# Performance work log

Measured on AMD Instinct MI355X. Metric: run time of the kernel, lower is better.

## Reference

```python
import jax, jax.numpy as jnp
import numpy as np

ALPHA = 0.2  # leaky relu slope
NEG_BIG = -9e15


def setup_inputs() -> dict:
    key = jax.random.key(0)
    k1, k2, k3, k4 = jax.random.split(key, 4)
    B, N, Fin, Fout = 8, 2048, 128, 128
    h = jax.random.normal(k1, (B, N, Fin), dtype=jnp.float32)
    adj = jax.random.randint(k2, (N, N), 0, 2, dtype=jnp.int32)
    # xavier_uniform with gain=1.414
    limW = 1.414 * np.sqrt(6.0 / (Fin + Fout))
    W = jax.random.uniform(k3, (Fin, Fout), minval=-limW, maxval=limW, dtype=jnp.float32)
    lima = 1.414 * np.sqrt(6.0 / (2 * Fout + 1))
    a = jax.random.uniform(k4, (2 * Fout, 1), minval=-lima, maxval=lima, dtype=jnp.float32)
    return {"h": h, "adj": adj, "W": W, "a": a}


def reference(h, adj, W, a):
    # Wh: [B, N, F]
    Wh = jnp.einsum("bnf,fo->bno", h, W)
    Fout = W.shape[1]
    a1, a2 = a[:Fout, 0], a[Fout:, 0]  # [F], [F]
    # Additive score decomposition (same math as concat trick):
    # e[b,i,j] = leakyrelu(Wh_i . a1 + Wh_j . a2)
    s1 = Wh @ a1  # [B, N] (source/query part)
    s2 = Wh @ a2  # [B, N] (target part)
    e = s1[:, :, None] + s2[:, None, :]  # [B, N, N]
    e = jnp.where(e > 0, e, ALPHA * e)   # leaky relu
    e = jnp.where(adj[None, :, :] > 0, e, NEG_BIG)
    attention = jax.nn.softmax(e, axis=2)  # [B, N, N]
    # dropout is identity in eval mode
    h_prime = jnp.einsum("bij,bjf->bif", attention, Wh)
    return h_prime
```

## Files before the change

### kernel.cpp

```cpp
#include <hip/hip_runtime.h>
#include <hip/hip_bf16.h>
#include <stdint.h>

#define ALPHA 0.2f

typedef __attribute__((ext_vector_type(8))) short bf16x8;
typedef __attribute__((ext_vector_type(4))) float f32x4;

__device__ __forceinline__ short f2bf(float f) {
    union { float f; uint32_t u; } c; c.f = f;
    uint32_t u = c.u + 0x7FFF + ((c.u >> 16) & 1);
    return (short)(u >> 16);
}

__device__ __forceinline__ uint32_t pk_bf16(float lo, float hi) {
    union { float f; uint32_t u; } a, b;
    a.f = lo; b.f = hi;
    return __builtin_amdgcn_perm(b.u + 0x8000u, a.u + 0x8000u, 0x07060302u);
}

__global__ __launch_bounds__(256) void pack_adj_kernel(
        const int* __restrict__ adj, uint8_t* __restrict__ bytes,
        const float* __restrict__ W, short* __restrict__ WTg) {
    int t = blockIdx.x * 256 + threadIdx.x;
    const int4* a4 = reinterpret_cast<const int4*>(adj) + (size_t)t * 2;
    int4 x0 = a4[0], x1 = a4[1];
    uint32_t m = 0;
    m |= (x0.x > 0) ? 1u   : 0u;  m |= (x0.y > 0) ? 2u   : 0u;
    m |= (x0.z > 0) ? 4u   : 0u;  m |= (x0.w > 0) ? 8u   : 0u;
    m |= (x1.x > 0) ? 16u  : 0u;  m |= (x1.y > 0) ? 32u  : 0u;
    m |= (x1.z > 0) ? 64u  : 0u;  m |= (x1.w > 0) ? 128u : 0u;
    bytes[t] = (uint8_t)m;

    if (blockIdx.x < 64) {
        int idx = blockIdx.x * 256 + threadIdx.x;
        int k = idx >> 7, f = idx & 127;
        WTg[f * 128 + k] = f2bf(W[k * 128 + f]);
    }
}

__global__ __launch_bounds__(256) void wh_kernel(
        const float* __restrict__ h, const short* __restrict__ WTg,
        const float* __restrict__ a, short* __restrict__ whT,
        float* __restrict__ s1g, float* __restrict__ s2g) {
    __shared__ float sred[4][2][16];
    __shared__ short tr[4][32][24];

    int tid = threadIdx.x, wid = tid >> 6, lane = tid & 63;
    int q = lane >> 4, n = lane & 15;
    int bb = blockIdx.x & 7;
    int tile = blockIdx.x >> 3;
    int rb = bb * 2048 + tile * 16;
    int row = rb + n;

    f32x4 acc[2] = {};
    #pragma unroll
    for (int kc = 0; kc < 4; ++kc) {
        const float* hp = h + (size_t)row * 128 + kc * 32 + q * 8;
        float4 h0 = reinterpret_cast<const float4*>(hp)[0];
        float4 h1 = reinterpret_cast<const float4*>(hp)[1];
        bf16x8 afrag;
        afrag[0] = f2bf(h0.x); afrag[1] = f2bf(h0.y);
        afrag[2] = f2bf(h0.z); afrag[3] = f2bf(h0.w);
        afrag[4] = f2bf(h1.x); afrag[5] = f2bf(h1.y);
        afrag[6] = f2bf(h1.z); afrag[7] = f2bf(h1.w);
        #pragma unroll
        for (int u = 0; u < 2; ++u) {
            int t = wid * 2 + u;
            bf16x8 bfrag = *reinterpret_cast<const bf16x8*>(
                WTg + (t * 16 + n) * 128 + kc * 32 + q * 8);
            acc[u] = __builtin_amdgcn_mfma_f32_16x16x32_bf16(afrag, bfrag, acc[u], 0, 0, 0);
        }
    }

    float p1[4] = {0.f, 0.f, 0.f, 0.f}, p2[4] = {0.f, 0.f, 0.f, 0.f};
    #pragma unroll
    for (int u = 0; u < 2; ++u) {
        int c = (wid * 2 + u) * 16 + n;
        float a1c = a[c], a2c = a[128 + c];
        #pragma unroll
        for (int r = 0; r < 4; ++r) {
            p1[r] += acc[u][r] * a1c;
            p2[r] += acc[u][r] * a2c;
        }
    }
    #pragma unroll
    for (int d = 1; d < 16; d <<= 1) {
        #pragma unroll
        for (int r = 0; r < 4; ++r) {
            p1[r] += __shfl_xor(p1[r], d);
            p2[r] += __shfl_xor(p2[r], d);
        }
    }
    if (n == 0) {
        #pragma unroll
        for (int r = 0; r < 4; ++r) {
            sred[wid][0][q * 4 + r] = p1[r];
            sred[wid][1][q * 4 + r] = p2[r];
        }
    }

    #pragma unroll
    for (int u = 0; u < 2; ++u)
        #pragma unroll
        for (int r = 0; r < 4; ++r)
            tr[wid][u * 16 + n][q * 4 + r] = f2bf(acc[u][r]);
    __syncthreads();

    if (wid == 0 && lane < 16) {
        float v1 = 0.f, v2 = 0.f;
        #pragma unroll
        for (int v = 0; v < 4; ++v) { v1 += sred[v][0][lane]; v2 += sred[v][1][lane]; }
        s1g[rb + lane] = v1;
        s2g[rb + lane] = v2;
    }

    int jr = rb & 2047;
    int fl = lane & 31, jh = lane >> 5;
    bf16x8 v = *reinterpret_cast<const bf16x8*>(&tr[wid][fl][jh * 8]);
    int f = wid * 32 + fl;
    int jc = jr >> 5, jo = (jr & 31) + jh * 8;
    *reinterpret_cast<bf16x8*>(
        whT + ((size_t)(bb * 64 + jc) * 128 + f) * 32 + jo) = v;
}

__global__ __launch_bounds__(256, 2) void attn_kernel(
        const short* __restrict__ whT, const float* __restrict__ s1g,
        const float* __restrict__ s2g, const uint8_t* __restrict__ adjb,
        float* __restrict__ out) {
    __shared__ f32x4 buf[4][8][64];
    __shared__ float lds_ds[4][2][16];

    int wid = threadIdx.x >> 6, lane = threadIdx.x & 63;
    int q = lane >> 4, n = lane & 15;
    int b  = blockIdx.x & 7;
    int ib = (blockIdx.x >> 3) * 32;
    int rowA = ib + n, rowB = rowA + 16;

    float s1A = s1g[b * 2048 + rowA];
    float s1B = s1g[b * 2048 + rowB];
    const float* s2b = s2g + b * 2048;

    int jbase = wid * 512;

    uint4 mregA = *reinterpret_cast<const uint4*>(
        adjb + (size_t)rowA * 256 + wid * 64 + q * 16);
    uint4 mregB = *reinterpret_cast<const uint4*>(
        adjb + (size_t)rowB * 256 + wid * 64 + q * 16);
    const uint32_t* mrA = reinterpret_cast<const uint32_t*>(&mregA);
    const uint32_t* mrB = reinterpret_cast<const uint32_t*>(&mregB);

    const short* bpn = whT + (size_t)b * 262144 + n * 32 + q * 8;

    f32x4 accA[8] = {}, accB[8] = {};
    float dsA = 0.f, dsB = 0.f;

    bf16x8 nb[2][8];
    float4 s2l[2], s2h[2];

    {
        int k0 = jbase;
        s2l[0] = *reinterpret_cast<const float4*>(s2b + k0 + q * 8);
        s2h[0] = *reinterpret_cast<const float4*>(s2b + k0 + q * 8 + 4);
        const short* bp = bpn + (size_t)(k0 >> 5) * 4096;
        #pragma unroll
        for (int t = 0; t < 8; ++t)
            nb[0][t] = *reinterpret_cast<const bf16x8*>(bp + t * 512);
    }

    #pragma unroll
    for (int c = 0; c < 16; ++c) {
        const int cur = c & 1, nxt = cur ^ 1;
        int k1 = jbase + ((c + 1) & 15) * 32;
        s2l[nxt] = *reinterpret_cast<const float4*>(s2b + k1 + q * 8);
        s2h[nxt] = *reinterpret_cast<const float4*>(s2b + k1 + q * 8 + 4);
        const short* bp = bpn + (size_t)(k1 >> 5) * 4096;
        #pragma unroll
        for (int t = 0; t < 8; ++t)
            nb[nxt][t] = *reinterpret_cast<const bf16x8*>(bp + t * 512);

        int srcl = (c >> 2) * 16 + n;
        uint32_t mAd = (uint32_t)__shfl((int)mrA[c & 3], srcl);
        uint32_t mBd = (uint32_t)__shfl((int)mrB[c & 3], srcl);
        uint32_t mA = mAd >> (q * 8);
        uint32_t mB = mBd >> (q * 8);

        float s2arr[8] = {s2l[cur].x, s2l[cur].y, s2l[cur].z, s2l[cur].w,
                          s2h[cur].x, s2h[cur].y, s2h[cur].z, s2h[cur].w};
        float pA[8], pB[8];
        #pragma unroll
        for (int j = 0; j < 8; ++j) {
            float eA = s1A + s2arr[j];
            eA = fmaxf(eA, ALPHA * eA);
            float vA = ((mA >> j) & 1) ? __expf(eA) : 0.0f;
            dsA += vA; pA[j] = vA;
            float eB = s1B + s2arr[j];
            eB = fmaxf(eB, ALPHA * eB);
            float vB = ((mB >> j) & 1) ? __expf(eB) : 0.0f;
            dsB += vB; pB[j] = vB;
        }
        union { uint32_t u[4]; bf16x8 v; } cvA, cvB;
        #pragma unroll
        for (int p = 0; p < 4; ++p) {
            cvA.u[p] = pk_bf16(pA[2 * p], pA[2 * p + 1]);
            cvB.u[p] = pk_bf16(pB[2 * p], pB[2 * p + 1]);
        }

        #pragma unroll
        for (int t = 0; t < 8; ++t) {
            accA[t] = __builtin_amdgcn_mfma_f32_16x16x32_bf16(cvA.v, nb[cur][t], accA[t], 0, 0, 0);
            accB[t] = __builtin_amdgcn_mfma_f32_16x16x32_bf16(cvB.v, nb[cur][t], accB[t], 0, 0, 0);
        }
    }

    dsA += __shfl_xor(dsA, 16); dsA += __shfl_xor(dsA, 32);
    dsB += __shfl_xor(dsB, 16); dsB += __shfl_xor(dsB, 32);
    if (q == 0) { lds_ds[wid][0][n] = dsA; lds_ds[wid][1][n] = dsB; }

    #pragma unroll
    for (int i = 0; i < 8; ++i) buf[wid][i][lane] = accA[i];
    __syncthreads();

    int t0 = wid * 2, t1 = wid * 2 + 1;
    f32x4 rA0 = buf[0][t0][lane] + buf[1][t0][lane] + buf[2][t0][lane] + buf[3][t0][lane];
    f32x4 rA1 = buf[0][t1][lane] + buf[1][t1][lane] + buf[2][t1][lane] + buf[3][t1][lane];

    float dAt = lds_ds[0][0][n] + lds_ds[1][0][n] + lds_ds[2][0][n] + lds_ds[3][0][n];
    float dBt = lds_ds[0][1][n] + lds_ds[1][1][n] + lds_ds[2][1][n] + lds_ds[3][1][n];
    float rdA[4], rdB[4];
    #pragma unroll
    for (int r = 0; r < 4; ++r) {
        rdA[r] = 1.0f / __shfl(dAt, q * 4 + r);
        rdB[r] = 1.0f / __shfl(dBt, q * 4 + r);
    }

    size_t ob = ((size_t)b * 2048 + ib) * 128;
    #pragma unroll
    for (int r = 0; r < 4; ++r) {
        out[ob + (size_t)(q * 4 + r) * 128 + t0 * 16 + n] = rA0[r] * rdA[r];
        out[ob + (size_t)(q * 4 + r) * 128 + t1 * 16 + n] = rA1[r] * rdA[r];
    }
    __syncthreads();

    #pragma unroll
    for (int i = 0; i < 8; ++i) buf[wid][i][lane] = accB[i];
    __syncthreads();

    f32x4 rB0 = buf[0][t0][lane] + buf[1][t0][lane] + buf[2][t0][lane] + buf[3][t0][lane];
    f32x4 rB1 = buf[0][t1][lane] + buf[1][t1][lane] + buf[2][t1][lane] + buf[3][t1][lane];
    #pragma unroll
    for (int r = 0; r < 4; ++r) {
        out[ob + (size_t)(16 + q * 4 + r) * 128 + t0 * 16 + n] = rB0[r] * rdB[r];
        out[ob + (size_t)(16 + q * 4 + r) * 128 + t1 * 16 + n] = rB1[r] * rdB[r];
    }
}

extern "C" void kernel_launch(void* const* d_in, const int* in_sizes, int n_in,
                              void* d_out, int out_size, void* d_ws, size_t ws_size,
                              hipStream_t stream) {
    const float* h   = (const float*)d_in[0];
    const int*   adj = (const int*)d_in[1];
    const float* W   = (const float*)d_in[2];
    const float* a   = (const float*)d_in[3];
    float* out = (float*)d_out;

    char* ws = (char*)d_ws;
    short* whT = (short*)ws;
    float* s1  = (float*)(ws + 4194304);
    float* s2  = (float*)(ws + 4259840);
    uint8_t* bytes = (uint8_t*)(ws + 4325376);

    short* WTg = (short*)d_out + (4194304 - 16384);

    pack_adj_kernel<<<2048, 256, 0, stream>>>(adj, bytes, W, WTg);
    wh_kernel<<<1024, 256, 0, stream>>>(h, WTg, a, whT, s1, s2);
    attn_kernel<<<512, 256, 0, stream>>>(whT, s1, s2, bytes, out);
}
```

Before: 111.7 us.

## Halve attention rows per block and preload s2 once via shuffles

The attention kernel now handles 16 query rows per block instead of 32 and launches twice as many blocks. Launch bounds are raised to allow 4 blocks per SM, and the per-chunk s2 global loads are replaced by one upfront load that is broadcast with lane shuffles. The aim is lower register pressure and higher occupancy. The cost is that each whT B-fragment load now feeds only one MFMA per tile instead of two, doubling B-operand traffic per output row.

```diff
diff --git a/kernel.cpp b/kernel.cpp
--- a/kernel.cpp
+++ b/kernel.cpp
@@ -124,45 +124,40 @@
         whT + ((size_t)(bb * 64 + jc) * 128 + f) * 32 + jo) = v;
 }
 
-__global__ __launch_bounds__(256, 2) void attn_kernel(
+__global__ __launch_bounds__(256, 4) void attn_kernel(
         const short* __restrict__ whT, const float* __restrict__ s1g,
         const float* __restrict__ s2g, const uint8_t* __restrict__ adjb,
         float* __restrict__ out) {
     __shared__ f32x4 buf[4][8][64];
-    __shared__ float lds_ds[4][2][16];
+    __shared__ float lds_ds[4][16];
 
     int wid = threadIdx.x >> 6, lane = threadIdx.x & 63;
     int q = lane >> 4, n = lane & 15;
     int b  = blockIdx.x & 7;
-    int ib = (blockIdx.x >> 3) * 32;
-    int rowA = ib + n, rowB = rowA + 16;
+    int ib = (blockIdx.x >> 3) * 16;
+    int rowA = ib + n;
 
     float s1A = s1g[b * 2048 + rowA];
-    float s1B = s1g[b * 2048 + rowB];
     const float* s2b = s2g + b * 2048;
-
     int jbase = wid * 512;
 
     uint4 mregA = *reinterpret_cast<const uint4*>(
         adjb + (size_t)rowA * 256 + wid * 64 + q * 16);
-    uint4 mregB = *reinterpret_cast<const uint4*>(
-        adjb + (size_t)rowB * 256 + wid * 64 + q * 16);
     const uint32_t* mrA = reinterpret_cast<const uint32_t*>(&mregA);
-    const uint32_t* mrB = reinterpret_cast<const uint32_t*>(&mregB);
+
+    float4 s2va = *reinterpret_cast<const float4*>(s2b + jbase + lane * 8);
+    float4 s2vb = *reinterpret_cast<const float4*>(s2b + jbase + lane * 8 + 4);
+    float s2v[8] = {s2va.x, s2va.y, s2va.z, s2va.w,
+                    s2vb.x, s2vb.y, s2vb.z, s2vb.w};
 
     const short* bpn = whT + (size_t)b * 262144 + n * 32 + q * 8;
 
-    f32x4 accA[8] = {}, accB[8] = {};
-    float dsA = 0.f, dsB = 0.f;
+    f32x4 accA[8] = {};
+    float dsA = 0.f;
 
     bf16x8 nb[2][8];
-    float4 s2l[2], s2h[2];
-
     {
-        int k0 = jbase;
-        s2l[0] = *reinterpret_cast<const float4*>(s2b + k0 + q * 8);
-        s2h[0] = *reinterpret_cast<const float4*>(s2b + k0 + q * 8 + 4);
-        const short* bp = bpn + (size_t)(k0 >> 5) * 4096;
+        const short* bp = bpn + (size_t)(jbase >> 5) * 4096;
         #pragma unroll
         for (int t = 0; t < 8; ++t)
             nb[0][t] = *reinterpret_cast<const bf16x8*>(bp + t * 512);
@@ -172,50 +167,39 @@
     for (int c = 0; c < 16; ++c) {
         const int cur = c & 1, nxt = cur ^ 1;
         int k1 = jbase + ((c + 1) & 15) * 32;
-        s2l[nxt] = *reinterpret_cast<const float4*>(s2b + k1 + q * 8);
-        s2h[nxt] = *reinterpret_cast<const float4*>(s2b + k1 + q * 8 + 4);
         const short* bp = bpn + (size_t)(k1 >> 5) * 4096;
         #pragma unroll
         for (int t = 0; t < 8; ++t)
             nb[nxt][t] = *reinterpret_cast<const bf16x8*>(bp + t * 512);
 
         int srcl = (c >> 2) * 16 + n;
-        uint32_t mAd = (uint32_t)__shfl((int)mrA[c & 3], srcl);
-        uint32_t mBd = (uint32_t)__shfl((int)mrB[c & 3], srcl);
-        uint32_t mA = mAd >> (q * 8);
-        uint32_t mB = mBd >> (q * 8);
-
-        float s2arr[8] = {s2l[cur].x, s2l[cur].y, s2l[cur].z, s2l[cur].w,
-                          s2h[cur].x, s2h[cur].y, s2h[cur].z, s2h[cur].w};
-        float pA[8], pB[8];
+        uint32_t mA = ((uint32_t)__shfl((int)mrA[c & 3], srcl)) >> (q * 8);
+
+        int s2src = c * 4 + q;
+        float s2arr[8];
+        #pragma unroll
+        for (int j = 0; j < 8; ++j) s2arr[j] = __shfl(s2v[j], s2src);
+
+        float pA[8];
         #pragma unroll
         for (int j = 0; j < 8; ++j) {
             float eA = s1A + s2arr[j];
             eA = fmaxf(eA, ALPHA * eA);
             float vA = ((mA >> j) & 1) ? __expf(eA) : 0.0f;
             dsA += vA; pA[j] = vA;
-            float eB = s1B + s2arr[j];
-            eB = fmaxf(eB, ALPHA * eB);
-            float vB = ((mB >> j) & 1) ? __expf(eB) : 0.0f;
-            dsB += vB; pB[j] = vB;
-        }
-        union { uint32_t u[4]; bf16x8 v; } cvA, cvB;
-        #pragma unroll
-        for (int p = 0; p < 4; ++p) {
+        }
+        union { uint32_t u[4]; bf16x8 v; } cvA;
+        #pragma unroll
+        for (int p = 0; p < 4; ++p)
             cvA.u[p] = pk_bf16(pA[2 * p], pA[2 * p + 1]);
-            cvB.u[p] = pk_bf16(pB[2 * p], pB[2 * p + 1]);
-        }
-
-        #pragma unroll
-        for (int t = 0; t < 8; ++t) {
+
+        #pragma unroll
+        for (int t = 0; t < 8; ++t)
             accA[t] = __builtin_amdgcn_mfma_f32_16x16x32_bf16(cvA.v, nb[cur][t], accA[t], 0, 0, 0);
-            accB[t] = __builtin_amdgcn_mfma_f32_16x16x32_bf16(cvB.v, nb[cur][t], accB[t], 0, 0, 0);
-        }
     }
 
     dsA += __shfl_xor(dsA, 16); dsA += __shfl_xor(dsA, 32);
-    dsB += __shfl_xor(dsB, 16); dsB += __shfl_xor(dsB, 32);
-    if (q == 0) { lds_ds[wid][0][n] = dsA; lds_ds[wid][1][n] = dsB; }
+    if (q == 0) lds_ds[wid][n] = dsA;
 
     #pragma unroll
     for (int i = 0; i < 8; ++i) buf[wid][i][lane] = accA[i];
@@ -225,33 +209,17 @@
     f32x4 rA0 = buf[0][t0][lane] + buf[1][t0][lane] + buf[2][t0][lane] + buf[3][t0][lane];
     f32x4 rA1 = buf[0][t1][lane] + buf[1][t1][lane] + buf[2][t1][lane] + buf[3][t1][lane];
 
-    float dAt = lds_ds[0][0][n] + lds_ds[1][0][n] + lds_ds[2][0][n] + lds_ds[3][0][n];
-    float dBt = lds_ds[0][1][n] + lds_ds[1][1][n] + lds_ds[2][1][n] + lds_ds[3][1][n];
-    float rdA[4], rdB[4];
-    #pragma unroll
-    for (int r = 0; r < 4; ++r) {
+    float dAt = lds_ds[0][n] + lds_ds[1][n] + lds_ds[2][n] + lds_ds[3][n];
+    float rdA[4];
+    #pragma unroll
+    for (int r = 0; r < 4; ++r)
         rdA[r] = 1.0f / __shfl(dAt, q * 4 + r);
-        rdB[r] = 1.0f / __shfl(dBt, q * 4 + r);
-    }
 
     size_t ob = ((size_t)b * 2048 + ib) * 128;
     #pragma unroll
     for (int r = 0; r < 4; ++r) {
         out[ob + (size_t)(q * 4 + r) * 128 + t0 * 16 + n] = rA0[r] * rdA[r];
         out[ob + (size_t)(q * 4 + r) * 128 + t1 * 16 + n] = rA1[r] * rdA[r];
-    }
-    __syncthreads();
-
-    #pragma unroll
-    for (int i = 0; i < 8; ++i) buf[wid][i][lane] = accB[i];
-    __syncthreads();
-
-    f32x4 rB0 = buf[0][t0][lane] + buf[1][t0][lane] + buf[2][t0][lane] + buf[3][t0][lane];
-    f32x4 rB1 = buf[0][t1][lane] + buf[1][t1][lane] + buf[2][t1][lane] + buf[3][t1][lane];
-    #pragma unroll
-    for (int r = 0; r < 4; ++r) {
-        out[ob + (size_t)(16 + q * 4 + r) * 128 + t0 * 16 + n] = rB0[r] * rdB[r];
-        out[ob + (size_t)(16 + q * 4 + r) * 128 + t1 * 16 + n] = rB1[r] * rdB[r];
     }
 }
 
@@ -274,5 +242,5 @@
 
     pack_adj_kernel<<<2048, 256, 0, stream>>>(adj, bytes, W, WTg);
     wh_kernel<<<1024, 256, 0, stream>>>(h, WTg, a, whT, s1, s2);
-    attn_kernel<<<512, 256, 0, stream>>>(whT, s1, s2, bytes, out);
-}
+    attn_kernel<<<1024, 256, 0, stream>>>(whT, s1, s2, bytes, out);
+}
```

Result: slower. 121.4 us (+8.7%).
